# Optimization experiments

Hardware: AMD Instinct MI355X
Metric: run time of the kernel (lower is better)

The kernel has to match this reference:

```python
import jax, jax.numpy as jnp
import numpy as np

WIDTH = 256   # image width == PSF_size in NeuWS
PSF = 256
BSZ = 16
PD = WIDTH // 2   # patch dim of each G_Tensor
NF = 32           # num_feats
NPE = 15          # 15 frequencies * 4 -> 60 PE basis channels


def _bilinear_coords(dim):
    # Reproduces G_FeatureTensor's precomputed bilinear lerp indices/weights (ds_factor=1).
    half = 0.5 / dim
    xs = np.linspace(half, 1.0 - half, dim, dtype=np.float64)
    xv, yv = np.meshgrid(xs, xs, indexing='ij')
    xy = np.stack([yv.ravel(), xv.ravel()], axis=1)        # (N, 2), cols = (y-like, x-like)
    s = (xy * dim).astype(np.float32)
    idx = s.astype(np.int64)
    lw = s - idx.astype(np.float32)
    x0 = np.clip(idx[:, 0], 0, dim - 1)
    y0 = np.clip(idx[:, 1], 0, dim - 1)
    x1 = np.minimum(x0 + 1, dim - 1)
    y1 = np.minimum(y0 + 1, dim - 1)
    return (jnp.asarray(lw), jnp.asarray(x0), jnp.asarray(y0),
            jnp.asarray(x1), jnp.asarray(y1))

_LW, _X0, _Y0, _X1, _Y1 = _bilinear_coords(PD)


def _sample(data):
    # data: [PD, PD, NF] -> [PD*PD, NF] bilinear gather (G_FeatureTensor.sample)
    lx, ly = _LW[:, 0:1], _LW[:, 1:2]
    return (data[_Y0, _X0] * (1.0 - lx) * (1.0 - ly)
            + data[_Y0, _X1] * lx * (1.0 - ly)
            + data[_Y1, _X0] * (1.0 - lx) * ly
            + data[_Y1, _X1] * lx * ly)


def _pe_basis():
    xs = np.linspace(-1.0, 1.0, PSF, dtype=np.float32)
    x, y = np.meshgrid(xs, xs, indexing='xy')
    feats = []
    for i in range(1, NPE + 1):
        feats += [np.sin(i * x), np.sin(i * y), np.cos(i * x), np.cos(i * y)]
    return jnp.asarray(np.stack(feats, axis=-1))           # [PSF, PSF, 60]

_BASIS = _pe_basis()


def _layernorm(x, w, b, eps=1e-5):
    m = x.mean(-1, keepdims=True)
    v = ((x - m) ** 2).mean(-1, keepdims=True)
    return (x - m) * jax.lax.rsqrt(v + eps) * w + b


def setup_inputs() -> dict:
    key = jax.random.key(0)
    ks = jax.random.split(key, 20)
    def n(k, shape, s=0.1):
        return s * jax.random.normal(k, shape, dtype=jnp.float32)
    return dict(
        x_batch=jax.random.normal(ks[0], (BSZ, 1, WIDTH, WIDTH), dtype=jnp.float32),
        t=jax.random.uniform(ks[1], (BSZ,), dtype=jnp.float32),
        patch_data=n(ks[2], (4, PD, PD, NF)),
        r_w0=n(ks[3], (4, NF, 32)), r_b0=n(ks[4], (4, 32)),
        r_w1=n(ks[5], (4, 32, 32)), r_b1=n(ks[6], (4, 32)),
        r_w2=n(ks[7], (4, 32, 1)), r_b2=n(ks[8], (4, 1)),
        g_w0=n(ks[9], (4 * NPE, 32)), g_b0=n(ks[10], (32,)),
        g_w1=n(ks[11], (32, 32)), g_b1=n(ks[12], (32,)),
        ln1_w=jnp.ones((32,), jnp.float32), ln1_b=jnp.zeros((32,), jnp.float32),
        g_w2=n(ks[13], (32, 32)), g_b2=n(ks[14], (32,)),
        ln2_w=jnp.ones((32,), jnp.float32), ln2_b=jnp.zeros((32,), jnp.float32),
        g_w3=n(ks[15], (32, 1)), g_b3=n(ks[16], (1,)),
    )


def reference(x_batch, t, patch_data, r_w0, r_b0, r_w1, r_b1, r_w2, r_b2,
              g_w0, g_b0, g_w1, g_b1, ln1_w, ln1_b, g_w2, g_b2, ln2_w, ln2_b,
              g_w3, g_b3):
    # ---- G_PatchTensor: 4 independent feature tensors + ReLU MLP renderers (vmapped)
    def patch(data, w0, b0, w1, b1, w2, b2):
        f = _sample(data)                                  # [PD*PD, NF]
        h = jax.nn.relu(f @ w0 + b0)
        h = jax.nn.relu(h @ w1 + b1)
        return (h @ w2 + b2).reshape(1, PD, PD)            # [1, PD, PD]
    p = jax.vmap(patch)(patch_data, r_w0, r_b0, r_w1, r_b1, r_w2, r_b2)  # [4,1,PD,PD]
    left = jnp.concatenate([p[0], p[1]], axis=-1)          # [1, PD, 2*PD]
    right = jnp.concatenate([p[2], p[3]], axis=-1)
    I_est = jnp.concatenate([left, right], axis=-2)[None]  # [1, 1, W, W]

    # ---- phase MLP g_g over the PE basis (static phase: no time channel)
    bsz = t.shape[0]
    g_in = jnp.broadcast_to(_BASIS, (bsz,) + _BASIS.shape)  # [B, PSF, PSF, 60]
    h = g_in @ g_w0 + g_b0
    h = jax.nn.leaky_relu(_layernorm(h @ g_w1 + g_b1, ln1_w, ln1_b))
    h = jax.nn.leaky_relu(_layernorm(h @ g_w2 + g_b2, ln2_w, ln2_b))
    sim_phs = jnp.transpose(h @ g_w3 + g_b3, (0, 3, 1, 2))  # [B, 1, PSF, PSF]
    sim_g = jnp.exp(1j * sim_phs)                            # complex64

    # ---- PSF synthesis: |fftshift(fft2(sim_g * x, norm='forward'))|^2, normalized, flipped
    field = sim_g * x_batch
    k = jnp.fft.fftshift(jnp.fft.fft2(field, norm='forward'), axes=(-2, -1))
    kernel = k.real ** 2 + k.imag ** 2
    kernel = kernel / kernel.sum(axis=(-2, -1), keepdims=True)
    kernel = kernel[:, :, ::-1, ::-1]

    size = I_est.shape[-1]
    Sf = jnp.fft.fft2(I_est, s=(2 * size, 2 * size))
    Kf = jnp.fft.fft2(kernel, s=(2 * size, 2 * size))
    y = jnp.fft.ifft2(Sf * Kf).real
    y = y[..., size // 2:-(size // 2), size // 2:-(size // 2)]  # [B, 1, W, W]
    return (jnp.squeeze(y), kernel, sim_g, sim_phs, I_est)
```

## Files before the change

### kernel.cpp

```cpp
#include <hip/hip_runtime.h>
#include <math.h>

__device__ float  g_norms[16];
__device__ float  g_partial[1024];
__device__ float  g_phs[65536];
__device__ float2 g_cs[65536];
__device__ float  g_Fx[256*32];
__device__ float  g_Gy[256*32];
__device__ float  g_I[65536];
__device__ float2 g_tw[512];
__device__ float2 g_SfA[256*512];
__device__ float2 g_Sf [512*512];
__device__ float2 g_F  [16*256*256];
__device__ float2 g_KA [8*256*512];
__device__ float2 g_P  [8*256*512];

__device__ __forceinline__ int rev4d8(int x){
  return ((x&3)<<6) | (((x>>2)&3)<<4) | (((x>>4)&3)<<2) | ((x>>6)&3);
}
__device__ __forceinline__ float2 cadd(float2 a, float2 b){ return make_float2(a.x+b.x, a.y+b.y); }
__device__ __forceinline__ float2 csub(float2 a, float2 b){ return make_float2(a.x-b.x, a.y-b.y); }
__device__ __forceinline__ float2 cmul(float2 a, float2 b){ return make_float2(a.x*b.x - a.y*b.y, a.x*b.y + a.y*b.x); }
__device__ __forceinline__ float2 cmulj(float2 a, float2 b){ return make_float2(a.x*b.x + a.y*b.y, a.y*b.x - a.x*b.y); }
__device__ __forceinline__ float2 addi(float2 a, float2 b){ return make_float2(a.x - b.y, a.y + b.x); }
__device__ __forceinline__ float2 subi(float2 a, float2 b){ return make_float2(a.x + b.y, a.y - b.x); }

#define LIDX(x) ((x) + ((x)>>2))
#define OUT_W(idx, val) do{ int _i = (idx); if ((unsigned)_i < (unsigned)osz) out[_i] = (val); }while(0)

__device__ __forceinline__ void mid4f_512(float* re, float* im, int r){
  #pragma unroll
  for (int q = 32; q >= 2; q >>= 2){
    __syncthreads();
    int k = r & (q-1);
    int base = ((r - k) << 2) + k;
    int a0=LIDX(base), a1=LIDX(base+q), a2=LIDX(base+2*q), a3=LIDX(base+3*q);
    float x0r=re[a0], x0i=im[a0], x1r=re[a1], x1i=im[a1];
    float x2r=re[a2], x2i=im[a2], x3r=re[a3], x3i=im[a3];
    float t0r=x0r+x2r, t0i=x0i+x2i, t1r=x0r-x2r, t1i=x0i-x2i;
    float t2r=x1r+x3r, t2i=x1i+x3i, t3r=x1r-x3r, t3i=x1i-x3i;
    float y0r=t0r+t2r, y0i=t0i+t2i, y2r=t0r-t2r, y2i=t0i-t2i;
    float y1r=t1r+t3i, y1i=t1i-t3r;
    float y3r=t1r-t3i, y3i=t1i+t3r;
    float2 w1=g_tw[2*q+k], w2=g_tw[q+k];
    float w3r=w1.x*w2.x-w1.y*w2.y, w3i=w1.x*w2.y+w1.y*w2.x;
    re[a0]=y0r; im[a0]=y0i;
    re[a1]=y1r*w1.x-y1i*w1.y; im[a1]=y1r*w1.y+y1i*w1.x;
    re[a2]=y2r*w2.x-y2i*w2.y; im[a2]=y2r*w2.y+y2i*w2.x;
    re[a3]=y3r*w3r-y3i*w3i;  im[a3]=y3r*w3i+y3i*w3r;
  }
  __syncthreads();
}

__device__ __forceinline__ void mid4i_512(float* re, float* im, int r){
  #pragma unroll
  for (int q = 2; q <= 32; q <<= 2){
    __syncthreads();
    int k = r & (q-1);
    int base = ((r - k) << 2) + k;
    int a0=LIDX(base), a1=LIDX(base+q), a2=LIDX(base+2*q), a3=LIDX(base+3*q);
    float z0r=re[a0], z0i=im[a0], z1r=re[a1], z1i=im[a1];
    float z2r=re[a2], z2i=im[a2], z3r=re[a3], z3i=im[a3];
    float2 w1=g_tw[2*q+k], w2=g_tw[q+k];
    float w3r=w1.x*w2.x-w1.y*w2.y, w3i=w1.x*w2.y+w1.y*w2.x;
    float b1r = z1r*w1.x + z1i*w1.y, b1i = z1i*w1.x - z1r*w1.y;
    float b2r = z2r*w2.x + z2i*w2.y, b2i = z2i*w2.x - z2r*w2.y;
    float b3r = z3r*w3r + z3i*w3i,  b3i = z3i*w3r - z3r*w3i;
    float u0r=z0r+b2r, u0i=z0i+b2i, u1r=z0r-b2r, u1i=z0i-b2i;
    float u2r=b1r+b3r, u2i=b1i+b3i, u3r=b1r-b3r, u3i=b1i-b3i;
    re[a0]=u0r+u2r; im[a0]=u0i+u2i;
    re[a1]=u1r-u3i; im[a1]=u1i+u3r;
    re[a2]=u0r-u2r; im[a2]=u0i-u2i;
    re[a3]=u1r+u3i; im[a3]=u1i-u3r;
  }
  __syncthreads();
}

__global__ __launch_bounds__(256) void k_L1(const float* __restrict__ gw0,
                                            const float* __restrict__ gb0,
                                            const float* __restrict__ x){
  int bid = blockIdx.x;
  if (bid < 66){
    int t = bid*256 + threadIdx.x;
    if (t < 512){
      if (t == 0){ g_tw[0] = make_float2(1.f, 0.f); return; }
      int h = 1 << (31 - __clz(t));
      int k = t - h;
      double a = -M_PI * (double)k / (double)h;
      g_tw[t] = make_float2((float)cos(a), (float)sin(a));
      return;
    }
    int t2 = t - 512;
    if (t2 >= 16384) return;
    int isG = t2 >> 13;
    int pos = (t2 >> 5) & 255;
    int ch = t2 & 31;
    float xx = (float)(-1.0 + (2.0 * pos) / 255.0);
    float s1, c1; sincosf(xx, &s1, &c1);
    float s = s1, c = c1;
    float acc = isG ? 0.f : gb0[ch];
    #pragma unroll
    for (int i = 1; i <= 15; i++){
      const float* wsin = gw0 + (4*(i-1) + isG)*32;
      const float* wcos = gw0 + (4*(i-1) + 2 + isG)*32;
      acc += s*wsin[ch] + c*wcos[ch];
      float ns = s*c1 + c*s1, nc = c*c1 - s*s1;
      s = ns; c = nc;
    }
    if (isG) g_Gy[pos*32 + ch] = acc;
    else     g_Fx[pos*32 + ch] = acc;
  } else {
    int b = bid - 66;
    int tid = threadIdx.x;
    float4 v = ((const float4*)x)[(size_t)b*256 + tid];
    float s = v.x*v.x + v.y*v.y + v.z*v.z + v.w*v.w;
    __shared__ float red[256];
    red[tid] = s; __syncthreads();
    for (int w = 128; w > 0; w >>= 1){ if (tid < w) red[tid] += red[tid+w]; __syncthreads(); }
    if (tid == 0) g_partial[b] = red[0];
  }
}

__device__ __forceinline__ void gmlp_body(int bid,
    const float* __restrict__ gw1, const float* __restrict__ gb1,
    const float* __restrict__ l1w, const float* __restrict__ l1b,
    const float* __restrict__ gw2, const float* __restrict__ gb2,
    const float* __restrict__ l2w, const float* __restrict__ l2b,
    const float* __restrict__ gw3, const float* __restrict__ gb3)
{
  int tid = threadIdx.x;
  int waveid = tid >> 6, lane = tid & 63;
  int group = lane >> 3, j8 = lane & 7;
  int p = bid*32 + waveid*8 + group;
  int r = p >> 8, c = p & 255;
  int cb = 4*j8;

  float4 F4 = *(const float4*)&g_Fx[c*32 + cb];
  float4 G4 = *(const float4*)&g_Gy[r*32 + cb];
  float h0[4] = {F4.x+G4.x, F4.y+G4.y, F4.z+G4.z, F4.w+G4.w};

  float4 b1v = *(const float4*)&gb1[cb];
  float h1[4] = {b1v.x, b1v.y, b1v.z, b1v.w};
  #pragma unroll
  for (int k = 0; k < 32; k++){
    float hk = __shfl(h0[k&3], k>>2, 8);
    float4 w = *(const float4*)&gw1[k*32 + cb];
    h1[0] += hk*w.x; h1[1] += hk*w.y; h1[2] += hk*w.z; h1[3] += hk*w.w;
  }
  {
    float s = h1[0]+h1[1]+h1[2]+h1[3];
    s += __shfl_xor(s,1,8); s += __shfl_xor(s,2,8); s += __shfl_xor(s,4,8);
    float mean = s*(1.0f/32.0f);
    float d0=h1[0]-mean, d1=h1[1]-mean, d2=h1[2]-mean, d3=h1[3]-mean;
    float vv = d0*d0+d1*d1+d2*d2+d3*d3;
    vv += __shfl_xor(vv,1,8); vv += __shfl_xor(vv,2,8); vv += __shfl_xor(vv,4,8);
    float inv = rsqrtf(vv*(1.0f/32.0f) + 1e-5f);
    float4 lw = *(const float4*)&l1w[cb];
    float4 lb = *(const float4*)&l1b[cb];
    float t0=d0*inv*lw.x+lb.x, t1=d1*inv*lw.y+lb.y, t2=d2*inv*lw.z+lb.z, t3=d3*inv*lw.w+lb.w;
    h1[0] = (t0>0.f)?t0:0.01f*t0; h1[1] = (t1>0.f)?t1:0.01f*t1;
    h1[2] = (t2>0.f)?t2:0.01f*t2; h1[3] = (t3>0.f)?t3:0.01f*t3;
  }

  float4 b2v = *(const float4*)&gb2[cb];
  float h2[4] = {b2v.x, b2v.y, b2v.z, b2v.w};
  #pragma unroll
  for (int k = 0; k < 32; k++){
    float hk = __shfl(h1[k&3], k>>2, 8);
    float4 w = *(const float4*)&gw2[k*32 + cb];
    h2[0] += hk*w.x; h2[1] += hk*w.y; h2[2] += hk*w.z; h2[3] += hk*w.w;
  }
  {
    float s = h2[0]+h2[1]+h2[2]+h2[3];
    s += __shfl_xor(s,1,8); s += __shfl_xor(s,2,8); s += __shfl_xor(s,4,8);
    float mean = s*(1.0f/32.0f);
    float d0=h2[0]-mean, d1=h2[1]-mean, d2=h2[2]-mean, d3=h2[3]-mean;
    float vv = d0*d0+d1*d1+d2*d2+d3*d3;
    vv += __shfl_xor(vv,1,8); vv += __shfl_xor(vv,2,8); vv += __shfl_xor(vv,4,8);
    float inv = rsqrtf(vv*(1.0f/32.0f) + 1e-5f);
    float4 lw = *(const float4*)&l2w[cb];
    float4 lb = *(const float4*)&l2b[cb];
    float t0=d0*inv*lw.x+lb.x, t1=d1*inv*lw.y+lb.y, t2=d2*inv*lw.z+lb.z, t3=d3*inv*lw.w+lb.w;
    h2[0] = (t0>0.f)?t0:0.01f*t0; h2[1] = (t1>0.f)?t1:0.01f*t1;
    h2[2] = (t2>0.f)?t2:0.01f*t2; h2[3] = (t3>0.f)?t3:0.01f*t3;
  }

  float4 w3v = *(const float4*)&gw3[cb];
  float pp = h2[0]*w3v.x + h2[1]*w3v.y + h2[2]*w3v.z + h2[3]*w3v.w;
  pp += __shfl_xor(pp,1,8); pp += __shfl_xor(pp,2,8); pp += __shfl_xor(pp,4,8);
  float phs = pp + gb3[0];

  if (j8 == 0){
    float sp, cp; sincosf(phs, &sp, &cp);
    g_phs[p] = phs;
    g_cs[p] = make_float2(cp, sp);
  }
}

__device__ __forceinline__ void patch_body(int bid,
    const float* __restrict__ pdata, const float* __restrict__ rw0, const float* __restrict__ rb0,
    const float* __restrict__ rw1, const float* __restrict__ rb1,
    const float* __restrict__ rw2, const float* __restrict__ rb2,
    float* out, int osz, int offIest)
{
  int tid = threadIdx.x;
  int waveid = tid >> 6, lane = tid & 63;
  int group = lane >> 3, j8 = lane & 7;
  int p = bid*32 + waveid*8 + group;
  int patch = p >> 14;
  int pl = p & 16383;
  int i = pl >> 7, jp = pl & 127;
  int i1 = min(i+1, 127), j1 = min(jp+1, 127);
  int cb = 4*j8;

  const float* base = pdata + (size_t)patch * 128*128*32;
  float4 a  = *(const float4*)&base[(i *128 + jp)*32 + cb];
  float4 b  = *(const float4*)&base[(i *128 + j1)*32 + cb];
  float4 cc = *(const float4*)&base[(i1*128 + jp)*32 + cb];
  float4 d  = *(const float4*)&base[(i1*128 + j1)*32 + cb];
  float f[4] = {0.25f*(a.x+b.x+cc.x+d.x), 0.25f*(a.y+b.y+cc.y+d.y),
                0.25f*(a.z+b.z+cc.z+d.z), 0.25f*(a.w+b.w+cc.w+d.w)};

  const float* w0 = rw0 + patch*1024;
  const float* w1 = rw1 + patch*1024;

  float4 b0v = *(const float4*)&rb0[patch*32 + cb];
  float h[4] = {b0v.x, b0v.y, b0v.z, b0v.w};
  #pragma unroll
  for (int k = 0; k < 32; k++){
    float fk = __shfl(f[k&3], k>>2, 8);
    float4 w = *(const float4*)&w0[k*32 + cb];
    h[0] += fk*w.x; h[1] += fk*w.y; h[2] += fk*w.z; h[3] += fk*w.w;
  }
  h[0]=fmaxf(h[0],0.f); h[1]=fmaxf(h[1],0.f); h[2]=fmaxf(h[2],0.f); h[3]=fmaxf(h[3],0.f);

  float4 b1v = *(const float4*)&rb1[patch*32 + cb];
  float g[4] = {b1v.x, b1v.y, b1v.z, b1v.w};
  #pragma unroll
  for (int k = 0; k < 32; k++){
    float hk = __shfl(h[k&3], k>>2, 8);
    float4 w = *(const float4*)&w1[k*32 + cb];
    g[0] += hk*w.x; g[1] += hk*w.y; g[2] += hk*w.z; g[3] += hk*w.w;
  }

  float4 w2v = *(const float4*)&rw2[patch*32 + cb];
  float o = fmaxf(g[0],0.f)*w2v.x + fmaxf(g[1],0.f)*w2v.y
          + fmaxf(g[2],0.f)*w2v.z + fmaxf(g[3],0.f)*w2v.w;
  o += __shfl_xor(o,1,8); o += __shfl_xor(o,2,8); o += __shfl_xor(o,4,8);
  o += rb2[patch];

  if (j8 == 0){
    int pr = (patch >> 1)*128 + i;
    int pc = (patch & 1)*128 + jp;
    g_I[pr*256 + pc] = o;
    OUT_W(offIest + pr*256 + pc, o);
  }
}

__device__ __forceinline__ void norm2_body(){
  int tid = threadIdx.x;
  int b = tid >> 4, l = tid & 15;
  float s = 0.f;
  #pragma unroll
  for (int j = 0; j < 4; j++) s += g_partial[b*64 + l + 16*j];
  #pragma unroll
  for (int d = 8; d > 0; d >>= 1) s += __shfl_down(s, d, 16);
  if (l == 0) g_norms[b] = 65536.0f * s;
}

__global__ __launch_bounds__(256) void k_L2(
    const float* __restrict__ gw1, const float* __restrict__ gb1,
    const float* __restrict__ l1w, const float* __restrict__ l1b,
    const float* __restrict__ gw2, const float* __restrict__ gb2,
    const float* __restrict__ l2w, const float* __restrict__ l2b,
    const float* __restrict__ gw3, const float* __restrict__ gb3,
    const float* __restrict__ pdata, const float* __restrict__ rw0, const float* __restrict__ rb0,
    const float* __restrict__ rw1, const float* __restrict__ rb1,
    const float* __restrict__ rw2, const float* __restrict__ rb2,
    float* out, int osz, int offIest)
{
  int bid = blockIdx.x;
  if (bid < 2048)      gmlp_body(bid, gw1, gb1, l1w, l1b, gw2, gb2, l2w, l2b, gw3, gb3);
  else if (bid < 4096) patch_body(bid-2048, pdata, rw0, rb0, rw1, rb1, rw2, rb2, out, osz, offIest);
  else                 norm2_body();
}

__device__ __forceinline__ void srow_body(int bid, float* sm){
  int t = threadIdx.x;
  int row = t >> 7, r = t & 127;
  int gr = bid*2 + row;
  float* rre = sm + row*640; float* rim = sm + 1280 + row*640;
  float A = g_I[gr*256 + r], B = g_I[gr*256 + r + 128];
  {
    float2 w1 = g_tw[256+r], w2 = g_tw[128+r];
    float w3r = w1.x*w2.x - w1.y*w2.y, w3i = w1.x*w2.y + w1.y*w2.x;
    float s = A + B, d = A - B;
    rre[LIDX(r)]     = s;                   rim[LIDX(r)]     = 0.f;
    rre[LIDX(r+128)] = A*w1.x + B*w1.y;     rim[LIDX(r+128)] = A*w1.y - B*w1.x;
    rre[LIDX(r+256)] = d*w2.x;              rim[LIDX(r+256)] = d*w2.y;
    rre[LIDX(r+384)] = A*w3r - B*w3i;       rim[LIDX(r+384)] = A*w3i + B*w3r;
  }
  mid4f_512(rre, rim, r);
  float2* Srow = &g_SfA[gr*512];
  #pragma unroll
  for (int h = 0; h < 2; h++){
    int g = r + 128*h;
    int a0 = LIDX(2*g), a1 = LIDX(2*g+1);
    float ar = rre[a0], ai = rim[a0], br = rre[a1], bi = rim[a1];
    *(float4*)&Srow[2*g] = make_float4(ar+br, ai+bi, ar-br, ai-bi);
  }
}

__device__ __forceinline__ void frow_body(int bid, const float* __restrict__ x, float* sm){
  int t = threadIdx.x;
  int row = t >> 6, l = t & 63;
  int gr = bid*4 + row;
  int b = gr >> 8, xr = gr & 255;
  float* rre = sm + row*320; float* rim = sm + 1280 + row*320;
  const float* xrow = x + ((size_t)b*256 + xr)*256;
  const float2* csrow = g_cs + xr*256;

  float x0r,x0i,x1r,x1i,x2r,x2i,x3r,x3i;
  { float xv=xrow[l];      float2 cs=csrow[l];      x0r=xv*cs.x; x0i=xv*cs.y; }
  { float xv=xrow[l+64];   float2 cs=csrow[l+64];   x1r=xv*cs.x; x1i=xv*cs.y; }
  { float xv=xrow[l+128];  float2 cs=csrow[l+128];  x2r=xv*cs.x; x2i=xv*cs.y; }
  { float xv=xrow[l+192];  float2 cs=csrow[l+192];  x3r=xv*cs.x; x3i=xv*cs.y; }
  {
    float t0r=x0r+x2r, t0i=x0i+x2i, t1r=x0r-x2r, t1i=x0i-x2i;
    float t2r=x1r+x3r, t2i=x1i+x3i, t3r=x1r-x3r, t3i=x1i-x3i;
    float y0r=t0r+t2r, y0i=t0i+t2i, y2r=t0r-t2r, y2i=t0i-t2i;
    float y1r=t1r+t3i, y1i=t1i-t3r;
    float y3r=t1r-t3i, y3i=t1i+t3r;
    float2 w1=g_tw[128+l], w2=g_tw[64+l];
    float w3r=w1.x*w2.x-w1.y*w2.y, w3i=w1.x*w2.y+w1.y*w2.x;
    rre[LIDX(l)]     = y0r;                     rim[LIDX(l)]     = y0i;
    rre[LIDX(l+64)]  = y1r*w1.x-y1i*w1.y;       rim[LIDX(l+64)]  = y1r*w1.y+y1i*w1.x;
    rre[LIDX(l+128)] = y2r*w2.x-y2i*w2.y;       rim[LIDX(l+128)] = y2r*w2.y+y2i*w2.x;
    rre[LIDX(l+192)] = y3r*w3r-y3i*w3i;         rim[LIDX(l+192)] = y3r*w3i+y3i*w3r;
  }
  #pragma unroll
  for (int q = 16; q >= 4; q >>= 2){
    __syncthreads();
    int k = l & (q-1);
    int base = ((l - k) << 2) + k;
    int a0=LIDX(base), a1=LIDX(base+q), a2=LIDX(base+2*q), a3=LIDX(base+3*q);
    float z0r=rre[a0], z0i=rim[a0], z1r=rre[a1], z1i=rim[a1];
    float z2r=rre[a2], z2i=rim[a2], z3r=rre[a3], z3i=rim[a3];
    float t0r=z0r+z2r, t0i=z0i+z2i, t1r=z0r-z2r, t1i=z0i-z2i;
    float t2r=z1r+z3r, t2i=z1i+z3i, t3r=z1r-z3r, t3i=z1i-z3i;
    float y0r=t0r+t2r, y0i=t0i+t2i, y2r=t0r-t2r, y2i=t0i-t2i;
    float y1r=t1r+t3i, y1i=t1i-t3r;
    float y3r=t1r-t3i, y3i=t1i+t3r;
    float2 w1=g_tw[2*q+k], w2=g_tw[q+k];
    float w3r=w1.x*w2.x-w1.y*w2.y, w3i=w1.x*w2.y+w1.y*w2.x;
    rre[a0]=y0r; rim[a0]=y0i;
    rre[a1]=y1r*w1.x-y1i*w1.y; rim[a1]=y1r*w1.y+y1i*w1.x;
    rre[a2]=y2r*w2.x-y2i*w2.y; rim[a2]=y2r*w2.y+y2i*w2.x;
    rre[a3]=y3r*w3r-y3i*w3i;  rim[a3]=y3r*w3i+y3i*w3r;
  }
  __syncthreads();
  {
    int a0=LIDX(4*l), a1=LIDX(4*l+1), a2=LIDX(4*l+2), a3=LIDX(4*l+3);
    float z0r=rre[a0], z0i=rim[a0], z1r=rre[a1], z1i=rim[a1];
    float z2r=rre[a2], z2i=rim[a2], z3r=rre[a3], z3i=rim[a3];
    float t0r=z0r+z2r, t0i=z0i+z2i, t1r=z0r-z2r, t1i=z0i-z2i;
    float t2r=z1r+z3r, t2i=z1i+z3i, t3r=z1r-z3r, t3i=z1i-z3i;
    float2* Frow = &g_F[((size_t)b*256 + xr)*256];
    Frow[rev4d8(4*l)]   = make_float2(t0r+t2r, t0i+t2i);
    Frow[rev4d8(4*l+1)] = make_float2(t1r+t3i, t1i-t3r);
    Frow[rev4d8(4*l+2)] = make_float2(t0r-t2r, t0i-t2i);
    Frow[rev4d8(4*l+3)] = make_float2(t1r-t3i, t1i+t3r);
  }
}

__device__ __forceinline__ void bcast_body(int bid, float* out, int osz, int offG, int offPhs, int interleaved){
  int idx = bid*256 + threadIdx.x;
  int p = idx & 65535, b = idx >> 16;
  float phs = g_phs[p];
  float2 cs = g_cs[p];
  OUT_W(offPhs + b*65536 + p, phs);
  if (interleaved){
    int gi = offG + 2*(b*65536 + p);
    if (gi + 1 < osz) *(float2*)(out + gi) = cs;
  } else {
    OUT_W(offG + b*65536 + p, cs.x);
  }
}

__global__ __launch_bounds__(256) void k_L3(const float* __restrict__ x, float* out, int osz,
                                            int offG, int offPhs, int interleaved){
  __shared__ float sm[2560];
  int bid = blockIdx.x;
  if (bid < 128)       srow_body(bid, sm);
  else if (bid < 1152) frow_body(bid-128, x, sm);
  else                 bcast_body(bid-1152, out, osz, offG, offPhs, interleaved);
}

__device__ __forceinline__ void fold512_load(const float2* src, float2* buf, int c, int rr){
  for (int i = rr; i < 128; i += 32){
    float2 a = src[(size_t)i*512];
    float2 b = src[(size_t)(i+128)*512];
    float2 w1 = g_tw[256+i], w2 = g_tw[128+i];
    float2 w3 = cmul(w1, w2);
    buf[i*9+c]       = cadd(a,b);
    buf[(i+128)*9+c] = cmul(subi(a,b), w1);
    buf[(i+256)*9+c] = cmul(csub(a,b), w2);
    buf[(i+384)*9+c] = cmul(addi(a,b), w3);
  }
}

__device__ __forceinline__ void dif4_stages_512(float2* buf, int c, int rr){
  #pragma unroll
  for (int q = 32; q >= 2; q >>= 2){
    __syncthreads();
    for (int g = rr; g < 128; g += 32){
      int k = g & (q-1);
      int base = ((g - k) << 2) + k;
      float2 x0 = buf[base*9+c], x1 = buf[(base+q)*9+c];
      float2 x2 = buf[(base+2*q)*9+c], x3 = buf[(base+3*q)*9+c];
      float2 t0=cadd(x0,x2), t1=csub(x0,x2), t2=cadd(x1,x3), t3=csub(x1,x3);
      float2 y0=cadd(t0,t2), y1=subi(t1,t3), y2=csub(t0,t2), y3=addi(t1,t3);
      float2 w1 = g_tw[2*q+k], w2 = g_tw[q+k];
      float2 w3 = cmul(w1,w2);
      buf[base*9+c]       = y0;
      buf[(base+q)*9+c]   = cmul(y1,w1);
      buf[(base+2*q)*9+c] = cmul(y2,w2);
      buf[(base+3*q)*9+c] = cmul(y3,w3);
    }
  }
}

__device__ __forceinline__ void scol_body(int bid, float2* buf){
  int v0 = bid << 3;
  int tid = threadIdx.x, c = tid & 7, rr = tid >> 3;
  int v = v0 + c;
  fold512_load(&g_SfA[v], buf, c, rr);
  dif4_stages_512(buf, c, rr);
  __syncthreads();
  for (int g = rr; g < 256; g += 32){
    int i0 = 2*g;
    float2 a = buf[i0*9+c], b = buf[(i0+1)*9+c];
    g_Sf[(size_t)i0*512 + v]     = cadd(a,b);
    g_Sf[(size_t)(i0+1)*512 + v] = csub(a,b);
  }
}

__device__ __forceinline__ void fcol_body(int bid, float2* buf, float* out, int osz, int offKer){
  int b = bid >> 5, v0 = (bid & 31) << 3;
  int tid = threadIdx.x, c = tid & 7, rr = tid >> 3;
  const float2* Fr = &g_F[(size_t)b*65536 + v0 + c];
  for (int r = rr; r < 256; r += 32) buf[r*9+c] = Fr[(size_t)r*256];
  #pragma unroll
  for (int q = 64; q >= 1; q >>= 2){
    __syncthreads();
    for (int g = rr; g < 64; g += 32){
      int k = g & (q-1);
      int base = ((g - k) << 2) + k;
      float2 x0 = buf[base*9+c], x1 = buf[(base+q)*9+c];
      float2 x2 = buf[(base+2*q)*9+c], x3 = buf[(base+3*q)*9+c];
      float2 t0=cadd(x0,x2), t1=csub(x0,x2), t2=cadd(x1,x3), t3=csub(x1,x3);
      float2 y0=cadd(t0,t2), y1=subi(t1,t3), y2=csub(t0,t2), y3=addi(t1,t3);
      if (q > 1){
        float2 w1 = g_tw[2*q+k], w2 = g_tw[q+k];
        float2 w3 = cmul(w1,w2);
        y1 = cmul(y1,w1); y2 = cmul(y2,w2); y3 = cmul(y3,w3);
      }
      buf[base*9+c]=y0; buf[(base+q)*9+c]=y1; buf[(base+2*q)*9+c]=y2; buf[(base+3*q)*9+c]=y3;
    }
  }
  __syncthreads();
  float invn = 1.0f / g_norms[b];
  int v = v0 + c;
  int e = (127 - v) & 255;
  for (int p = rr; p < 256; p += 32){
    float2 f = buf[p*9+c];
    int a = rev4d8(p);
    int rt = (127 - a) & 255;
    float kv = (f.x*f.x + f.y*f.y) * invn;
    OUT_W(offKer + b*65536 + rt*256 + e, kv);
  }
}

__global__ __launch_bounds__(256) void k_L4(float* out, int osz, int offKer){
  __shared__ float2 buf[512*9];
  int bid = blockIdx.x;
  if (bid < 64) scol_body(bid, buf);
  else          fcol_body(bid-64, buf, out, osz, offKer);
}

__global__ __launch_bounds__(256) void k_krow(const float* __restrict__ out_ro, int osz, int offKer){
  __shared__ float re[2*640], im[2*640];
  int t = threadIdx.x;
  int row = t >> 7, r = t & 127;
  int gr = blockIdx.x*2 + row;
  int q = gr >> 8, kr = gr & 255;
  int b0 = 2*q, b1 = 2*q + 1;
  float* rre = re + row*640; float* rim = im + row*640;

  const float* k0 = out_ro + offKer + b0*65536 + kr*256;
  const float* k1 = out_ro + offKer + b1*65536 + kr*256;
  float2 zA = make_float2(k0[r],      k1[r]);
  float2 zB = make_float2(k0[r+128],  k1[r+128]);

  {
    float2 w1 = g_tw[256+r], w2 = g_tw[128+r];
    float2 w3 = cmul(w1, w2);
    float2 p0 = cadd(zA, zB);
    float2 p1 = cmul(subi(zA, zB), w1);
    float2 p2 = cmul(csub(zA, zB), w2);
    float2 p3 = cmul(addi(zA, zB), w3);
    rre[LIDX(r)]     = p0.x; rim[LIDX(r)]     = p0.y;
    rre[LIDX(r+128)] = p1.x; rim[LIDX(r+128)] = p1.y;
    rre[LIDX(r+256)] = p2.x; rim[LIDX(r+256)] = p2.y;
    rre[LIDX(r+384)] = p3.x; rim[LIDX(r+384)] = p3.y;
  }
  mid4f_512(rre, rim, r);
  float2* KArow = &g_KA[((size_t)q*256 + kr)*512];
  #pragma unroll
  for (int h = 0; h < 2; h++){
    int g = r + 128*h;
    int a0 = LIDX(2*g), a1 = LIDX(2*g+1);
    float ar = rre[a0], ai = rim[a0], br = rre[a1], bi = rim[a1];
    *(float4*)&KArow[2*g] = make_float4(ar+br, ai+bi, ar-br, ai-bi);
  }
}

__global__ __launch_bounds__(256) void k_col_mul_inv(){
  __shared__ float2 buf[512*9];
  int bi = blockIdx.x >> 6, v0 = (blockIdx.x & 63) << 3;
  int tid = threadIdx.x, c = tid & 7, rr = tid >> 3;
  int v = v0 + c;

  fold512_load(&g_KA[((size_t)bi*256)*512 + v], buf, c, rr);
  dif4_stages_512(buf, c, rr);

  __syncthreads();
  for (int g = rr; g < 256; g += 32){
    int i0 = 2*g;
    float2 a = buf[i0*9+c], b = buf[(i0+1)*9+c];
    float2 y0 = cadd(a,b), y1 = csub(a,b);
    float2 s0 = g_Sf[(size_t)i0*512 + v];
    float2 s1 = g_Sf[(size_t)(i0+1)*512 + v];
    float2 z0 = cmul(y0,s0), z1 = cmul(y1,s1);
    buf[i0*9+c]     = cadd(z0,z1);
    buf[(i0+1)*9+c] = csub(z0,z1);
  }

  #pragma unroll
  for (int q = 2; q <= 32; q <<= 2){
    __syncthreads();
    for (int g = rr; g < 128; g += 32){
      int k = g & (q-1);
      int base = ((g - k) << 2) + k;
      float2 z0 = buf[base*9+c], z1 = buf[(base+q)*9+c];
      float2 z2 = buf[(base+2*q)*9+c], z3 = buf[(base+3*q)*9+c];
      float2 w1 = g_tw[2*q+k], w2 = g_tw[q+k];
      float2 w3 = cmul(w1,w2);
      z1 = cmulj(z1,w1); z2 = cmulj(z2,w2); z3 = cmulj(z3,w3);
      float2 u0=cadd(z0,z2), u1=csub(z0,z2), u2=cadd(z1,z3), u3=csub(z1,z3);
      buf[base*9+c]       = cadd(u0,u2);
      buf[(base+q)*9+c]   = addi(u1,u3);
      buf[(base+2*q)*9+c] = csub(u0,u2);
      buf[(base+3*q)*9+c] = subi(u1,u3);
    }
  }

  __syncthreads();
  for (int i = rr; i < 128; i += 32){
    float2 z0 = buf[i*9+c], z1 = buf[(i+128)*9+c];
    float2 z2 = buf[(i+256)*9+c], z3 = buf[(i+384)*9+c];
    float2 w1 = g_tw[256+i], w2 = g_tw[128+i];
    float2 w3 = cmul(w1,w2);
    z1 = cmulj(z1,w1); z2 = cmulj(z2,w2); z3 = cmulj(z3,w3);
    float2 u0=cadd(z0,z2), u1=csub(z0,z2), u2=cadd(z1,z3), u3=csub(z1,z3);
    g_P[((size_t)bi*256 + i)*512 + v]       = addi(u1,u3);
    g_P[((size_t)bi*256 + i + 128)*512 + v] = csub(u0,u2);
  }
}

__global__ __launch_bounds__(256) void k_ifft_row(float* out, int osz){
  __shared__ float re[2*640], im[2*640];
  int t = threadIdx.x;
  int row = t >> 7, r = t & 127;
  int gr = blockIdx.x*2 + row;
  int q = gr >> 8, ri = gr & 255;
  int b0 = 2*q, b1 = 2*q + 1;
  float* rre = re + row*640; float* rim = im + row*640;
  const float2* Prow = &g_P[((size_t)q*256 + ri)*512];

  #pragma unroll
  for (int h = 0; h < 2; h++){
    int g = r + 128*h;
    float4 pq = *(const float4*)&Prow[2*g];
    rre[LIDX(2*g)]   = pq.x + pq.z;  rim[LIDX(2*g)]   = pq.y + pq.w;
    rre[LIDX(2*g+1)] = pq.x - pq.z;  rim[LIDX(2*g+1)] = pq.y - pq.w;
  }
  mid4i_512(rre, rim, r);
  {
    int a0=LIDX(r), a1=LIDX(r+128), a2=LIDX(r+256), a3=LIDX(r+384);
    float z0r=rre[a0], z0i=rim[a0];
    float z1r=rre[a1], z1i=rim[a1];
    float z2r=rre[a2], z2i=rim[a2];
    float z3r=rre[a3], z3i=rim[a3];
    float2 w1 = g_tw[256+r], w2 = g_tw[128+r];
    float w3r=w1.x*w2.x-w1.y*w2.y, w3i=w1.x*w2.y+w1.y*w2.x;
    float b1r = z1r*w1.x + z1i*w1.y, b1i = z1i*w1.x - z1r*w1.y;
    float b2r = z2r*w2.x + z2i*w2.y, b2i = z2i*w2.x - z2r*w2.y;
    float b3r = z3r*w3r + z3i*w3i,  b3i = z3i*w3r - z3r*w3i;
    float u0r = z0r + b2r, u0i = z0i + b2i;
    float u1r = z0r - b2r, u1i = z0i - b2i;
    float u2r = b1r + b3r, u2i = b1i + b3i;
    float u3r = b1r - b3r, u3i = b1i - b3i;
    const float sc = 1.0f / 262144.0f;
    OUT_W(b0*65536 + ri*256 + r,       (u1r - u3i) * sc);
    OUT_W(b1*65536 + ri*256 + r,       (u1i + u3r) * sc);
    OUT_W(b0*65536 + ri*256 + r + 128, (u0r - u2r) * sc);
    OUT_W(b1*65536 + ri*256 + r + 128, (u0i - u2i) * sc);
  }
}

extern "C" void kernel_launch(void* const* d_in, const int* in_sizes, int n_in,
                              void* d_out, int out_size, void* d_ws, size_t ws_size,
                              hipStream_t stream) {
  static const int expect[21] = {
    16*65536, 16, 4*128*128*32,
    4*32*32, 4*32, 4*32*32, 4*32, 4*32, 4,
    60*32, 32, 32*32, 32, 32, 32, 32*32, 32, 32, 32, 32, 1
  };
  if (n_in < 21) return;
  for (int i = 0; i < 21; i++) if (in_sizes[i] != expect[i]) return;

  const float* x_batch = (const float*)d_in[0];
  const float* pdata = (const float*)d_in[2];
  const float* rw0 = (const float*)d_in[3];
  const float* rb0 = (const float*)d_in[4];
  const float* rw1 = (const float*)d_in[5];
  const float* rb1 = (const float*)d_in[6];
  const float* rw2 = (const float*)d_in[7];
  const float* rb2 = (const float*)d_in[8];
  const float* gw0 = (const float*)d_in[9];
  const float* gb0 = (const float*)d_in[10];
  const float* gw1 = (const float*)d_in[11];
  const float* gb1 = (const float*)d_in[12];
  const float* l1w = (const float*)d_in[13];
  const float* l1b = (const float*)d_in[14];
  const float* gw2 = (const float*)d_in[15];
  const float* gb2 = (const float*)d_in[16];
  const float* l2w = (const float*)d_in[17];
  const float* l2b = (const float*)d_in[18];
  const float* gw3 = (const float*)d_in[19];
  const float* gb3 = (const float*)d_in[20];

  float* out = (float*)d_out;

  int interleaved = (out_size >= 5308416) ? 1 : 0;
  int offKer  = 1048576;
  int offG    = 2097152;
  int offPhs  = interleaved ? 4194304 : 3145728;
  int offIest = interleaved ? 5242880 : 4194304;

  k_L1<<<1090, 256, 0, stream>>>(gw0, gb0, x_batch);
  k_L2<<<4097, 256, 0, stream>>>(gw1, gb1, l1w, l1b, gw2, gb2, l2w, l2b, gw3, gb3,
                                 pdata, rw0, rb0, rw1, rb1, rw2, rb2, out, out_size, offIest);
  k_L3<<<5248, 256, 0, stream>>>(x_batch, out, out_size, offG, offPhs, interleaved);
  k_L4<<<576, 256, 0, stream>>>(out, out_size, offKer);
  k_krow<<<1024, 256, 0, stream>>>(out, out_size, offKer);
  k_col_mul_inv<<<512, 256, 0, stream>>>();
  k_ifft_row<<<1024, 256, 0, stream>>>(out, out_size);
}
```

Baseline: 89.52 us.

## Map one pixel per thread in MLP stages with pre-transposed weights

The per-pixel MLPs (the phase-mask G network and the patch-feature network) move from an 8-lanes-per-pixel layout with shuffles to one thread per pixel, holding the 32-wide hidden vectors in registers. Weight matrices are transposed into global scratch buffers in k_L1 so each output neuron reads a contiguous row, and the weight loads become uniform across the wavefront. This removes the cross-lane shuffle traffic and cuts the k_L2 grid from 4097 to 513 blocks. In exchange, register pressure rises (arrays of 32 floats) and there are far fewer blocks, which may lower occupancy and latency hiding.

```diff
diff --git a/kernel.cpp b/kernel.cpp
--- a/kernel.cpp
+++ b/kernel.cpp
@@ -8,6 +8,10 @@
 __device__ float  g_Fx[256*32];
 __device__ float  g_Gy[256*32];
 __device__ float  g_I[65536];
+__device__ float  g_W1t[1024];
+__device__ float  g_W2t[1024];
+__device__ float  g_R0t[4096];
+__device__ float  g_R1t[4096];
 __device__ float2 g_tw[512];
 __device__ float2 g_SfA[256*512];
 __device__ float2 g_Sf [512*512];
@@ -78,6 +82,10 @@
 
 __global__ __launch_bounds__(256) void k_L1(const float* __restrict__ gw0,
                                             const float* __restrict__ gb0,
+                                            const float* __restrict__ gw1,
+                                            const float* __restrict__ gw2,
+                                            const float* __restrict__ rw0,
+                                            const float* __restrict__ rw1,
                                             const float* __restrict__ x){
   int bid = blockIdx.x;
   if (bid < 66){
@@ -109,7 +117,7 @@
     }
     if (isG) g_Gy[pos*32 + ch] = acc;
     else     g_Fx[pos*32 + ch] = acc;
-  } else {
+  } else if (bid < 1090) {
     int b = bid - 66;
     int tid = threadIdx.x;
     float4 v = ((const float4*)x)[(size_t)b*256 + tid];
@@ -118,143 +126,171 @@
     red[tid] = s; __syncthreads();
     for (int w = 128; w > 0; w >>= 1){ if (tid < w) red[tid] += red[tid+w]; __syncthreads(); }
     if (tid == 0) g_partial[b] = red[0];
+  } else {
+    int t = (bid - 1090)*256 + threadIdx.x;
+    if (t < 1024){
+      g_W1t[t] = gw1[(t & 31)*32 + (t >> 5)];
+    } else if (t < 2048){
+      int u = t - 1024;
+      g_W2t[u] = gw2[(u & 31)*32 + (u >> 5)];
+    } else if (t < 6144){
+      int u = t - 2048;
+      int patch = u >> 10, v = u & 1023;
+      g_R0t[patch*1024 + v] = rw0[patch*1024 + (v & 31)*32 + (v >> 5)];
+    } else {
+      int u = t - 6144;
+      int patch = u >> 10, v = u & 1023;
+      g_R1t[patch*1024 + v] = rw1[patch*1024 + (v & 31)*32 + (v >> 5)];
+    }
   }
 }
 
 __device__ __forceinline__ void gmlp_body(int bid,
-    const float* __restrict__ gw1, const float* __restrict__ gb1,
-    const float* __restrict__ l1w, const float* __restrict__ l1b,
-    const float* __restrict__ gw2, const float* __restrict__ gb2,
-    const float* __restrict__ l2w, const float* __restrict__ l2b,
+    const float* __restrict__ gb1, const float* __restrict__ l1w, const float* __restrict__ l1b,
+    const float* __restrict__ gb2, const float* __restrict__ l2w, const float* __restrict__ l2b,
     const float* __restrict__ gw3, const float* __restrict__ gb3)
 {
   int tid = threadIdx.x;
-  int waveid = tid >> 6, lane = tid & 63;
-  int group = lane >> 3, j8 = lane & 7;
-  int p = bid*32 + waveid*8 + group;
+  int p = bid*256 + tid;
   int r = p >> 8, c = p & 255;
-  int cb = 4*j8;
-
-  float4 F4 = *(const float4*)&g_Fx[c*32 + cb];
-  float4 G4 = *(const float4*)&g_Gy[r*32 + cb];
-  float h0[4] = {F4.x+G4.x, F4.y+G4.y, F4.z+G4.z, F4.w+G4.w};
-
-  float4 b1v = *(const float4*)&gb1[cb];
-  float h1[4] = {b1v.x, b1v.y, b1v.z, b1v.w};
-  #pragma unroll
-  for (int k = 0; k < 32; k++){
-    float hk = __shfl(h0[k&3], k>>2, 8);
-    float4 w = *(const float4*)&gw1[k*32 + cb];
-    h1[0] += hk*w.x; h1[1] += hk*w.y; h1[2] += hk*w.z; h1[3] += hk*w.w;
+
+  float h0[32];
+  #pragma unroll
+  for (int q = 0; q < 8; q++){
+    float4 F4 = *(const float4*)&g_Fx[c*32 + 4*q];
+    float4 G4 = *(const float4*)&g_Gy[r*32 + 4*q];
+    h0[4*q+0]=F4.x+G4.x; h0[4*q+1]=F4.y+G4.y; h0[4*q+2]=F4.z+G4.z; h0[4*q+3]=F4.w+G4.w;
+  }
+
+  float h1[32];
+  #pragma unroll
+  for (int j = 0; j < 32; j++){
+    const float* wr = &g_W1t[j*32];
+    float a0=0.f, a1=0.f, a2=0.f, a3=0.f;
+    #pragma unroll
+    for (int k = 0; k < 32; k += 4){
+      a0 += h0[k+0]*wr[k+0]; a1 += h0[k+1]*wr[k+1];
+      a2 += h0[k+2]*wr[k+2]; a3 += h0[k+3]*wr[k+3];
+    }
+    h1[j] = gb1[j] + (a0+a1) + (a2+a3);
   }
   {
-    float s = h1[0]+h1[1]+h1[2]+h1[3];
-    s += __shfl_xor(s,1,8); s += __shfl_xor(s,2,8); s += __shfl_xor(s,4,8);
+    float s = 0.f;
+    #pragma unroll
+    for (int j = 0; j < 32; j++) s += h1[j];
     float mean = s*(1.0f/32.0f);
-    float d0=h1[0]-mean, d1=h1[1]-mean, d2=h1[2]-mean, d3=h1[3]-mean;
-    float vv = d0*d0+d1*d1+d2*d2+d3*d3;
-    vv += __shfl_xor(vv,1,8); vv += __shfl_xor(vv,2,8); vv += __shfl_xor(vv,4,8);
+    float vv = 0.f;
+    #pragma unroll
+    for (int j = 0; j < 32; j++){ float d = h1[j]-mean; vv += d*d; }
     float inv = rsqrtf(vv*(1.0f/32.0f) + 1e-5f);
-    float4 lw = *(const float4*)&l1w[cb];
-    float4 lb = *(const float4*)&l1b[cb];
-    float t0=d0*inv*lw.x+lb.x, t1=d1*inv*lw.y+lb.y, t2=d2*inv*lw.z+lb.z, t3=d3*inv*lw.w+lb.w;
-    h1[0] = (t0>0.f)?t0:0.01f*t0; h1[1] = (t1>0.f)?t1:0.01f*t1;
-    h1[2] = (t2>0.f)?t2:0.01f*t2; h1[3] = (t3>0.f)?t3:0.01f*t3;
-  }
-
-  float4 b2v = *(const float4*)&gb2[cb];
-  float h2[4] = {b2v.x, b2v.y, b2v.z, b2v.w};
-  #pragma unroll
-  for (int k = 0; k < 32; k++){
-    float hk = __shfl(h1[k&3], k>>2, 8);
-    float4 w = *(const float4*)&gw2[k*32 + cb];
-    h2[0] += hk*w.x; h2[1] += hk*w.y; h2[2] += hk*w.z; h2[3] += hk*w.w;
+    #pragma unroll
+    for (int j = 0; j < 32; j++){
+      float t = (h1[j]-mean)*inv*l1w[j] + l1b[j];
+      h1[j] = (t > 0.f) ? t : 0.01f*t;
+    }
+  }
+
+  float h2[32];
+  #pragma unroll
+  for (int j = 0; j < 32; j++){
+    const float* wr = &g_W2t[j*32];
+    float a0=0.f, a1=0.f, a2=0.f, a3=0.f;
+    #pragma unroll
+    for (int k = 0; k < 32; k += 4){
+      a0 += h1[k+0]*wr[k+0]; a1 += h1[k+1]*wr[k+1];
+      a2 += h1[k+2]*wr[k+2]; a3 += h1[k+3]*wr[k+3];
+    }
+    h2[j] = gb2[j] + (a0+a1) + (a2+a3);
   }
   {
-    float s = h2[0]+h2[1]+h2[2]+h2[3];
-    s += __shfl_xor(s,1,8); s += __shfl_xor(s,2,8); s += __shfl_xor(s,4,8);
+    float s = 0.f;
+    #pragma unroll
+    for (int j = 0; j < 32; j++) s += h2[j];
     float mean = s*(1.0f/32.0f);
-    float d0=h2[0]-mean, d1=h2[1]-mean, d2=h2[2]-mean, d3=h2[3]-mean;
-    float vv = d0*d0+d1*d1+d2*d2+d3*d3;
-    vv += __shfl_xor(vv,1,8); vv += __shfl_xor(vv,2,8); vv += __shfl_xor(vv,4,8);
+    float vv = 0.f;
+    #pragma unroll
+    for (int j = 0; j < 32; j++){ float d = h2[j]-mean; vv += d*d; }
     float inv = rsqrtf(vv*(1.0f/32.0f) + 1e-5f);
-    float4 lw = *(const float4*)&l2w[cb];
-    float4 lb = *(const float4*)&l2b[cb];
-    float t0=d0*inv*lw.x+lb.x, t1=d1*inv*lw.y+lb.y, t2=d2*inv*lw.z+lb.z, t3=d3*inv*lw.w+lb.w;
-    h2[0] = (t0>0.f)?t0:0.01f*t0; h2[1] = (t1>0.f)?t1:0.01f*t1;
-    h2[2] = (t2>0.f)?t2:0.01f*t2; h2[3] = (t3>0.f)?t3:0.01f*t3;
-  }
-
-  float4 w3v = *(const float4*)&gw3[cb];
-  float pp = h2[0]*w3v.x + h2[1]*w3v.y + h2[2]*w3v.z + h2[3]*w3v.w;
-  pp += __shfl_xor(pp,1,8); pp += __shfl_xor(pp,2,8); pp += __shfl_xor(pp,4,8);
-  float phs = pp + gb3[0];
-
-  if (j8 == 0){
-    float sp, cp; sincosf(phs, &sp, &cp);
-    g_phs[p] = phs;
-    g_cs[p] = make_float2(cp, sp);
-  }
+    #pragma unroll
+    for (int j = 0; j < 32; j++){
+      float t = (h2[j]-mean)*inv*l2w[j] + l2b[j];
+      h2[j] = (t > 0.f) ? t : 0.01f*t;
+    }
+  }
+
+  float phs = gb3[0];
+  #pragma unroll
+  for (int j = 0; j < 32; j++) phs += h2[j]*gw3[j];
+
+  float sp, cp; sincosf(phs, &sp, &cp);
+  g_phs[p] = phs;
+  g_cs[p] = make_float2(cp, sp);
 }
 
 __device__ __forceinline__ void patch_body(int bid,
-    const float* __restrict__ pdata, const float* __restrict__ rw0, const float* __restrict__ rb0,
-    const float* __restrict__ rw1, const float* __restrict__ rb1,
-    const float* __restrict__ rw2, const float* __restrict__ rb2,
+    const float* __restrict__ pdata, const float* __restrict__ rb0,
+    const float* __restrict__ rb1, const float* __restrict__ rw2, const float* __restrict__ rb2,
     float* out, int osz, int offIest)
 {
   int tid = threadIdx.x;
-  int waveid = tid >> 6, lane = tid & 63;
-  int group = lane >> 3, j8 = lane & 7;
-  int p = bid*32 + waveid*8 + group;
-  int patch = p >> 14;
+  int patch = bid >> 6;
+  int p = bid*256 + tid;
   int pl = p & 16383;
   int i = pl >> 7, jp = pl & 127;
   int i1 = min(i+1, 127), j1 = min(jp+1, 127);
-  int cb = 4*j8;
 
   const float* base = pdata + (size_t)patch * 128*128*32;
-  float4 a  = *(const float4*)&base[(i *128 + jp)*32 + cb];
-  float4 b  = *(const float4*)&base[(i *128 + j1)*32 + cb];
-  float4 cc = *(const float4*)&base[(i1*128 + jp)*32 + cb];
-  float4 d  = *(const float4*)&base[(i1*128 + j1)*32 + cb];
-  float f[4] = {0.25f*(a.x+b.x+cc.x+d.x), 0.25f*(a.y+b.y+cc.y+d.y),
-                0.25f*(a.z+b.z+cc.z+d.z), 0.25f*(a.w+b.w+cc.w+d.w)};
-
-  const float* w0 = rw0 + patch*1024;
-  const float* w1 = rw1 + patch*1024;
-
-  float4 b0v = *(const float4*)&rb0[patch*32 + cb];
-  float h[4] = {b0v.x, b0v.y, b0v.z, b0v.w};
-  #pragma unroll
-  for (int k = 0; k < 32; k++){
-    float fk = __shfl(f[k&3], k>>2, 8);
-    float4 w = *(const float4*)&w0[k*32 + cb];
-    h[0] += fk*w.x; h[1] += fk*w.y; h[2] += fk*w.z; h[3] += fk*w.w;
-  }
-  h[0]=fmaxf(h[0],0.f); h[1]=fmaxf(h[1],0.f); h[2]=fmaxf(h[2],0.f); h[3]=fmaxf(h[3],0.f);
-
-  float4 b1v = *(const float4*)&rb1[patch*32 + cb];
-  float g[4] = {b1v.x, b1v.y, b1v.z, b1v.w};
-  #pragma unroll
-  for (int k = 0; k < 32; k++){
-    float hk = __shfl(h[k&3], k>>2, 8);
-    float4 w = *(const float4*)&w1[k*32 + cb];
-    g[0] += hk*w.x; g[1] += hk*w.y; g[2] += hk*w.z; g[3] += hk*w.w;
-  }
-
-  float4 w2v = *(const float4*)&rw2[patch*32 + cb];
-  float o = fmaxf(g[0],0.f)*w2v.x + fmaxf(g[1],0.f)*w2v.y
-          + fmaxf(g[2],0.f)*w2v.z + fmaxf(g[3],0.f)*w2v.w;
-  o += __shfl_xor(o,1,8); o += __shfl_xor(o,2,8); o += __shfl_xor(o,4,8);
-  o += rb2[patch];
-
-  if (j8 == 0){
-    int pr = (patch >> 1)*128 + i;
-    int pc = (patch & 1)*128 + jp;
-    g_I[pr*256 + pc] = o;
-    OUT_W(offIest + pr*256 + pc, o);
-  }
+  float f[32];
+  #pragma unroll
+  for (int q = 0; q < 8; q++){
+    float4 a  = *(const float4*)&base[(i *128 + jp)*32 + 4*q];
+    float4 b  = *(const float4*)&base[(i *128 + j1)*32 + 4*q];
+    float4 cc = *(const float4*)&base[(i1*128 + jp)*32 + 4*q];
+    float4 d  = *(const float4*)&base[(i1*128 + j1)*32 + 4*q];
+    f[4*q+0] = 0.25f*(a.x+b.x+cc.x+d.x);
+    f[4*q+1] = 0.25f*(a.y+b.y+cc.y+d.y);
+    f[4*q+2] = 0.25f*(a.z+b.z+cc.z+d.z);
+    f[4*q+3] = 0.25f*(a.w+b.w+cc.w+d.w);
+  }
+
+  const float* W0 = &g_R0t[patch*1024];
+  const float* W1 = &g_R1t[patch*1024];
+  const float* b0p = rb0 + patch*32;
+  const float* b1p = rb1 + patch*32;
+  const float* w2p = rw2 + patch*32;
+
+  float h[32];
+  #pragma unroll
+  for (int j = 0; j < 32; j++){
+    const float* wr = &W0[j*32];
+    float a0=0.f, a1=0.f, a2=0.f, a3=0.f;
+    #pragma unroll
+    for (int k = 0; k < 32; k += 4){
+      a0 += f[k+0]*wr[k+0]; a1 += f[k+1]*wr[k+1];
+      a2 += f[k+2]*wr[k+2]; a3 += f[k+3]*wr[k+3];
+    }
+    float t = b0p[j] + (a0+a1) + (a2+a3);
+    h[j] = fmaxf(t, 0.f);
+  }
+
+  float o = rb2[patch];
+  #pragma unroll
+  for (int j = 0; j < 32; j++){
+    const float* wr = &W1[j*32];
+    float a0=0.f, a1=0.f, a2=0.f, a3=0.f;
+    #pragma unroll
+    for (int k = 0; k < 32; k += 4){
+      a0 += h[k+0]*wr[k+0]; a1 += h[k+1]*wr[k+1];
+      a2 += h[k+2]*wr[k+2]; a3 += h[k+3]*wr[k+3];
+    }
+    float g = b1p[j] + (a0+a1) + (a2+a3);
+    o += fmaxf(g, 0.f) * w2p[j];
+  }
+
+  int pr = (patch >> 1)*128 + i;
+  int pc = (patch & 1)*128 + jp;
+  g_I[pr*256 + pc] = o;
+  OUT_W(offIest + pr*256 + pc, o);
 }
 
 __device__ __forceinline__ void norm2_body(){
@@ -269,20 +305,17 @@
 }
 
 __global__ __launch_bounds__(256) void k_L2(
-    const float* __restrict__ gw1, const float* __restrict__ gb1,
-    const float* __restrict__ l1w, const float* __restrict__ l1b,
-    const float* __restrict__ gw2, const float* __restrict__ gb2,
-    const float* __restrict__ l2w, const float* __restrict__ l2b,
+    const float* __restrict__ gb1, const float* __restrict__ l1w, const float* __restrict__ l1b,
+    const float* __restrict__ gb2, const float* __restrict__ l2w, const float* __restrict__ l2b,
     const float* __restrict__ gw3, const float* __restrict__ gb3,
-    const float* __restrict__ pdata, const float* __restrict__ rw0, const float* __restrict__ rb0,
-    const float* __restrict__ rw1, const float* __restrict__ rb1,
-    const float* __restrict__ rw2, const float* __restrict__ rb2,
+    const float* __restrict__ pdata, const float* __restrict__ rb0,
+    const float* __restrict__ rb1, const float* __restrict__ rw2, const float* __restrict__ rb2,
     float* out, int osz, int offIest)
 {
   int bid = blockIdx.x;
-  if (bid < 2048)      gmlp_body(bid, gw1, gb1, l1w, l1b, gw2, gb2, l2w, l2b, gw3, gb3);
-  else if (bid < 4096) patch_body(bid-2048, pdata, rw0, rb0, rw1, rb1, rw2, rb2, out, osz, offIest);
-  else                 norm2_body();
+  if (bid < 256)      gmlp_body(bid, gb1, l1w, l1b, gb2, l2w, l2b, gw3, gb3);
+  else if (bid < 512) patch_body(bid-256, pdata, rb0, rb1, rw2, rb2, out, osz, offIest);
+  else                norm2_body();
 }
 
 __device__ __forceinline__ void srow_body(int bid, float* sm){
@@ -659,9 +692,9 @@
   int offPhs  = interleaved ? 4194304 : 3145728;
   int offIest = interleaved ? 5242880 : 4194304;
 
-  k_L1<<<1090, 256, 0, stream>>>(gw0, gb0, x_batch);
-  k_L2<<<4097, 256, 0, stream>>>(gw1, gb1, l1w, l1b, gw2, gb2, l2w, l2b, gw3, gb3,
-                                 pdata, rw0, rb0, rw1, rb1, rw2, rb2, out, out_size, offIest);
+  k_L1<<<1130, 256, 0, stream>>>(gw0, gb0, gw1, gw2, rw0, rw1, x_batch);
+  k_L2<<<513, 256, 0, stream>>>(gb1, l1w, l1b, gb2, l2w, l2b, gw3, gb3,
+                                pdata, rb0, rb1, rw2, rb2, out, out_size, offIest);
   k_L3<<<5248, 256, 0, stream>>>(x_batch, out, out_size, offG, offPhs, interleaved);
   k_L4<<<576, 256, 0, stream>>>(out, out_size, offKer);
   k_krow<<<1024, 256, 0, stream>>>(out, out_size, offKer);
```

Result: slower. 136.4 us (+52.3%).
